# Optimization experiments

Hardware: AMD Instinct MI355X
Metric: run time of the kernel (lower is better)

The kernel has to match this reference:

```python
import jax, jax.numpy as jnp
import numpy as np

N_EVENTS = 200_000
M_TYPES = 64
K_KERNELS = 4
T_VAL = 100.0


def setup_inputs() -> dict:
    key = jax.random.key(0)
    k1, k2, k3, k4, k5 = jax.random.split(key, 5)
    # sorted event times in (0, T)
    t = jnp.sort(jax.random.uniform(k1, (N_EVENTS,), dtype=jnp.float32)) * T_VAL
    ti = t.reshape(1, N_EVENTS, 1)
    mi = jax.random.randint(k2, (N_EVENTS,), 0, M_TYPES)
    # positive Hawkes parameters (stability: row sums of alpha < 1)
    mu = 0.1 + 0.5 * jax.random.uniform(k3, (M_TYPES,), dtype=jnp.float32)
    alpha = (0.5 / M_TYPES) * jax.random.uniform(k4, (K_KERNELS, M_TYPES, M_TYPES), dtype=jnp.float32)
    gamma = 0.5 + jax.random.uniform(k5, (K_KERNELS,), dtype=jnp.float32)
    return {"mu": mu, "alpha": alpha, "gamma": gamma, "ti": ti, "mi": mi, "T": 100}


def _decay_states(gamma, t, mi, M):
    """Prefix-scan states h[i, m', k] = exp(-gamma_k*dt_i) * (h[i-1, m', k] + 1{m_{i-1}=m'}).
    Matches alpha_transition_matrices / prefix_scan(state_mult) in HawkesNLL.backward."""
    dt = jnp.concatenate([jnp.zeros((1,), t.dtype), t[1:] - t[:-1]])          # (N,)
    decay = jnp.exp(-gamma[None, :] * dt[:, None])                            # (N, K)
    oh = jnp.concatenate([jnp.zeros((1, M), t.dtype),
                          jax.nn.one_hot(mi[:-1], M, dtype=t.dtype)], axis=0)  # (N, M)
    a = jnp.broadcast_to(decay[:, None, :], (t.shape[0], M, decay.shape[1]))  # (N, M, K)
    b = decay[:, None, :] * oh[:, :, None]                                    # (N, M, K)

    def combine(x, y):
        a1, b1 = x
        a2, b2 = y
        return a1 * a2, a2 * b1 + b2

    _, h = jax.lax.associative_scan(combine, (a, b), axis=0)
    return h                                                                  # (N, M, K)


def _nll(mu, alpha, gamma, ti, mi, T):
    t = ti.reshape(-1)                        # (N,)
    N = t.shape[0]
    M = alpha.shape[1]
    h = _decay_states(gamma, t, mi, M)        # (N, M, K)
    # intensity at each event: lam_i = mu[m_i] + sum_{k,m'} gamma_k * alpha[k, m', m_i] * h[i, m', k]
    lam = mu[mi] + jnp.einsum('kmn,nmk,k->n', alpha[:, :, mi], h, gamma)      # (N,)
    # compensator: T*sum(mu) + sum_{j,k,p} alpha[k, m_j, p] * (1 - exp(-gamma_k (T - t_j)))
    asum = alpha.sum(axis=2)                                                  # (K, M)
    surv = -jnp.expm1(-gamma[None, :] * (T - t)[:, None])                     # (N, K)
    comp = T * mu.sum() + jnp.sum(asum[:, mi].T * surv)
    return (-jnp.sum(jnp.log(lam)) + comp) / N


def reference(mu, alpha, gamma, ti, mi, T):
    return _nll(mu, alpha, gamma, ti, mi, jnp.float32(T))
```

## Files before the change

kernel.cpp:

```cpp
#include <hip/hip_runtime.h>

#define MT 64
#define KK 4
#define NBK 4096
#define MAXB 49

__device__ __forceinline__ float wredf(float v) {
  #pragma unroll
  for (int off = 32; off > 0; off >>= 1) v += __shfl_xor(v, off, 64);
  return v;
}
__device__ __forceinline__ double wredd(double v) {
  #pragma unroll
  for (int off = 32; off > 0; off >>= 1) v += __shfl_xor(v, off, 64);
  return v;
}
__device__ __forceinline__ float4 f4fma(float4 a, float4 b, float4 c) {
  return make_float4(fmaf(a.x,b.x,c.x), fmaf(a.y,b.y,c.y),
                     fmaf(a.z,b.z,c.z), fmaf(a.w,b.w,c.w));
}
__device__ __forceinline__ float4 f4mul(float4 a, float4 b) {
  return make_float4(a.x*b.x, a.y*b.y, a.z*b.z, a.w*b.w);
}
__device__ __forceinline__ float parse_T(const int* Tp) {
  int v = *Tp;
  if (v >= 1 && v <= 1000000000) return (float)v;
  return __int_as_float(v);
}

__global__ __launch_bounds__(512, 4) void k_phase1(
    const float* __restrict__ t, const int* __restrict__ mi,
    const float* __restrict__ alpha, const float* __restrict__ gamma,
    const int* __restrict__ Tp,
    float4* __restrict__ cd4G, float* __restrict__ slG,
    float4* __restrict__ Cl8, float4* __restrict__ Dc8,
    float4* __restrict__ Ag, float4* __restrict__ gdec,
    float* __restrict__ compP, int N, int B)
{
  __shared__ float4 AT4[MT*MT];
  __shared__ __align__(16) unsigned char pool[8320];
  __shared__ float sL[8*MAXB];
  __shared__ float4 asumS[MT];
  __shared__ float red[8];
  float4*        d4t = (float4*)pool;
  unsigned char* miL = pool + 8*MAXB*16;
  float4*        cw  = (float4*)pool;
  float4*        cwd = (float4*)(pool + 8192);

  const int tid = threadIdx.x, lane = tid & 63, wv = tid >> 6;
  const float g0=gamma[0], g1=gamma[1], g2=gamma[2], g3=gamma[3];

  #pragma unroll
  for (int idx = tid; idx < MT*MT; idx += 512) {
    float a0=alpha[idx],         a1=alpha[MT*MT+idx];
    float a2=alpha[2*MT*MT+idx], a3=alpha[3*MT*MT+idx];
    AT4[idx] = make_float4(g0*a0, g1*a1, g2*a2, g3*a3);
  }
  if (tid < MT*KK) {
    const int m = tid >> 2, k = tid & 3;
    const float4* row = (const float4*)(alpha + (size_t)k*MT*MT + m*MT);
    float s = 0.f;
    #pragma unroll
    for (int j = 0; j < MT/4; ++j) { float4 v = row[j]; s += (v.x+v.y)+(v.z+v.w); }
    ((float*)asumS)[(m<<2)+k] = s;
  }
  __syncthreads();

  const float T = parse_T(Tp);
  const int s0w = (int)blockIdx.x * 8 * B;
  const int b  = (int)blockIdx.x*8 + wv;
  const int s0 = b*B, e0 = min(N, s0+B);
  float4 q = make_float4(0.f,0.f,0.f,0.f);
  float comp = 0.f;
  const int nch = (B + MAXB - 1) / MAXB;

  for (int ch = 0; ch < nch; ++ch) {
    const int c0 = ch*MAXB;
    const int cb = min(B - c0, MAXB);
    const int tot = 8*cb;
    for (int jj = tid; jj < tot; jj += 512) {
      int w = jj / cb, lo = jj - w*cb;
      int i = s0w + w*B + c0 + lo;
      if (i < N) {
        float ti = t[i];
        float tp = (i > 0) ? t[i-1] : ti;
        float dt = ti - tp;
        d4t[jj] = make_float4(__expf(-g0*dt), __expf(-g1*dt),
                              __expf(-g2*dt), __expf(-g3*dt));
        int m = mi[i];
        miL[jj] = (unsigned char)m;
        int refi = s0w + w*B - 1;
        float tr = (refi >= 0) ? t[refi] : t[0];
        float x = ti - tr;
        cd4G[i] = make_float4(__expf(-g0*x), __expf(-g1*x),
                              __expf(-g2*x), __expf(-g3*x));
        float y = T - ti;
        float4 as = asumS[m];
        comp = fmaf(as.x, 1.f-__expf(-g0*y), comp);
        comp = fmaf(as.y, 1.f-__expf(-g1*y), comp);
        comp = fmaf(as.z, 1.f-__expf(-g2*y), comp);
        comp = fmaf(as.w, 1.f-__expf(-g3*y), comp);
      }
    }
    __syncthreads();
    const int iend = min(cb, e0 - s0 - c0);
    int j = wv*cb;
    #pragma unroll 4
    for (int ii = 0; ii < iend; ++ii, ++j) {
      float4 d = d4t[j];
      int m = miL[j];
      float4 a = AT4[(m<<6) + lane];
      float s = q.x*d.x; s=fmaf(q.y,d.y,s); s=fmaf(q.z,d.z,s); s=fmaf(q.w,d.w,s);
      if (lane == m) sL[j] = s;
      q = f4fma(q, d, a);
    }
    __syncthreads();
    for (int jj = tid; jj < tot; jj += 512) {
      int w = jj / cb, lo = jj - w*cb;
      int i = s0w + w*B + c0 + lo;
      if (i < N) slG[i] = sL[jj];
    }
    __syncthreads();
  }

  comp = wredf(comp);
  if (lane == 0) red[wv] = comp;

  float4 df = make_float4(1.f,1.f,1.f,1.f);
  if (lane == 0) {
    int last  = max(e0-1, 0);
    int plast = min(max(s0-1, 0), N-1);
    float dtb = t[last] - t[plast];
    df = make_float4(__expf(-g0*dtb),__expf(-g1*dtb),
                     __expf(-g2*dtb),__expf(-g3*dtb));
  }
  cw[wv*64 + lane] = q;
  if (lane == 0) cwd[wv] = df;
  __syncthreads();

  float4 c  = make_float4(0.f,0.f,0.f,0.f);
  float4 dp = make_float4(1.f,1.f,1.f,1.f);
  float4 Cl = c, Dc = dp;
  #pragma unroll
  for (int jo = 0; jo < 8; ++jo) {
    if (jo == wv) { Cl = c; Dc = dp; }
    float4 d = cwd[jo];
    float4 P = cw[jo*64 + lane];
    c  = f4fma(c, d, P);
    dp = f4mul(dp, d);
  }
  Cl8[(size_t)b*64 + lane] = Cl;
  if (lane == 0) Dc8[b] = Dc;
  if (wv == 0) {
    Ag[(size_t)blockIdx.x*64 + lane] = c;
    if (lane == 0) gdec[blockIdx.x] = dp;
    if (lane == 0) {
      float cc = 0.f;
      #pragma unroll
      for (int jr = 0; jr < 8; ++jr) cc += red[jr];
      compP[blockIdx.x] = cc;
    }
  }
}

__global__ __launch_bounds__(64) void k_scan2(
    const float4* __restrict__ Ag, const float4* __restrict__ gdec,
    float4* __restrict__ SgG, float4* __restrict__ sdecG)
{
  const int lane = threadIdx.x;
  const int s = blockIdx.x;
  float4 c  = make_float4(0.f,0.f,0.f,0.f);
  float4 dp = make_float4(1.f,1.f,1.f,1.f);
  #pragma unroll 8
  for (int j = 0; j < 32; ++j) {
    const int o = s*32 + j;
    float4 gd = gdec[o];
    float4 a  = Ag[(size_t)o*64 + lane];
    c  = f4fma(c, gd, a);
    dp = f4mul(dp, gd);
  }
  SgG[(size_t)s*64 + lane] = c;
  if (lane == 0) sdecG[s] = dp;
}

__global__ __launch_bounds__(512, 4) void k_lam(
    const int* __restrict__ mi, const float* __restrict__ mu,
    const float4* __restrict__ cd4G, const float* __restrict__ slG,
    const float4* __restrict__ Cl8, const float4* __restrict__ Dc8,
    const float4* __restrict__ Ag, const float4* __restrict__ gdec,
    const float4* __restrict__ SgG, const float4* __restrict__ sdecG,
    float* __restrict__ npt, int N, int B)
{
  __shared__ float4 TopL[64];
  __shared__ float4 gpL[64];
  __shared__ float4 gdLs;
  __shared__ float red[8];
  const int tid = threadIdx.x, lane = tid & 63, wv = tid >> 6;
  const int oct = blockIdx.x;
  const int sup = oct >> 5;

  if (wv == 0) {
    float4 tc = make_float4(0.f,0.f,0.f,0.f);
    for (int s = 0; s < sup; ++s)
      tc = f4fma(tc, sdecG[s], SgG[(size_t)s*64 + lane]);
    TopL[lane] = tc;
  } else if (wv == 1) {
    float4 gp = make_float4(0.f,0.f,0.f,0.f);
    float4 gd = make_float4(1.f,1.f,1.f,1.f);
    const int o0 = sup << 5;
    for (int o = o0; o < oct; ++o) {
      gp = f4fma(gp, gdec[o], Ag[(size_t)o*64 + lane]);
      gd = f4mul(gd, gdec[o]);
    }
    gpL[lane] = gp;
    if (lane == 0) gdLs = gd;
  }
  __syncthreads();

  const int BPW = 8*B;
  const int i = oct*BPW + tid;
  float v = 0.f;
  if (tid < BPW && i < N) {
    int m = mi[i];
    float4 cd = cd4G[i];
    float sl = slG[i];
    int bl = tid / B;
    int b = oct*8 + bl;
    float4 coct = f4fma(gdLs, TopL[m], gpL[m]);
    float4 C = f4fma(Dc8[b], coct, Cl8[(size_t)b*64 + m]);
    float lam = mu[m] + sl + (C.x*cd.x + C.y*cd.y + C.z*cd.z + C.w*cd.w);
    v = __log2f(lam);
  }
  v = wredf(v);
  if (lane == 0) red[wv] = v;
  __syncthreads();
  if (tid == 0) {
    float s = 0.f;
    #pragma unroll
    for (int j = 0; j < 8; ++j) s += red[j];
    npt[oct] = s;
  }
}

__global__ __launch_bounds__(512) void k_final(
    const float* __restrict__ mu, const int* __restrict__ Tp,
    const float* __restrict__ compP, int nc,
    const float* __restrict__ npt, int nn,
    float* __restrict__ out, int N)
{
  const int tid = threadIdx.x;
  double sc = 0.0, sn = 0.0;
  for (int i = tid; i < nc; i += 512) sc += (double)compP[i];
  for (int i = tid; i < nn; i += 512) sn += (double)npt[i];
  double sm = (tid < MT) ? (double)mu[tid] : 0.0;
  sc = wredd(sc); sn = wredd(sn); sm = wredd(sm);
  __shared__ double s3[3][8];
  const int wv = tid >> 6, lane = tid & 63;
  if (lane == 0) { s3[0][wv]=sc; s3[1][wv]=sn; s3[2][wv]=sm; }
  __syncthreads();
  if (tid == 0) {
    double C=0.0, L=0.0, Mm=0.0;
    #pragma unroll
    for (int j = 0; j < 8; ++j) { C+=s3[0][j]; L+=s3[1][j]; Mm+=s3[2][j]; }
    L *= 0.6931471805599453;
    double T = (double)parse_T(Tp);
    out[0] = (float)((C + T*Mm - L) / (double)N);
  }
}

extern "C" void kernel_launch(void* const* d_in, const int* in_sizes, int n_in,
                              void* d_out, int out_size, void* d_ws, size_t ws_size,
                              hipStream_t stream)
{
  const float* mu    = (const float*)d_in[0];
  const float* alpha = (const float*)d_in[1];
  const float* gamma = (const float*)d_in[2];
  const float* t     = (const float*)d_in[3];
  const int*   mi    = (const int*)d_in[4];
  const int*   Tp    = (const int*)d_in[5];
  const int N = in_sizes[3];
  const int B   = (N + NBK - 1) / NBK;
  const int NOG = NBK / 8;

  float* p = (float*)d_ws;
  float4* cd4G  = (float4*)p; p += (size_t)N*4;
  float*  slG   = p;          p += ((size_t)N + 3) & ~(size_t)3;
  float4* Cl8   = (float4*)p; p += (size_t)NBK*256;
  float4* Dc8   = (float4*)p; p += (size_t)NBK*4;
  float4* Ag    = (float4*)p; p += (size_t)NOG*256;
  float4* gdec  = (float4*)p; p += (size_t)NOG*4;
  float4* SgG   = (float4*)p; p += (size_t)16*256;
  float4* sdecG = (float4*)p; p += (size_t)16*4;
  float*  compP = p;          p += NOG;
  float*  npt   = p;          p += NOG;

  k_phase1<<<NOG, 512, 0, stream>>>(t, mi, alpha, gamma, Tp, cd4G, slG,
                                    Cl8, Dc8, Ag, gdec, compP, N, B);
  k_scan2 <<<16,  64,  0, stream>>>(Ag, gdec, SgG, sdecG);
  k_lam   <<<NOG, 512, 0, stream>>>(mi, mu, cd4G, slG, Cl8, Dc8, Ag, gdec,
                                    SgG, sdecG, npt, N, B);
  k_final <<<1,   512, 0, stream>>>(mu, Tp, compP, NOG, npt, NOG,
                                    (float*)d_out, N);
}
```

Before: 37.64 us.

## Fuse scan2 and final reduction into lambda kernel with last-block atomic finish

Removes the separate small scan kernel by having every lambda block redundantly compute the super-block prefix sums into shared memory. The final reduction kernel is also folded in: blocks atomically add their log sums into a double accumulator, and the last block (found through an atomic counter) reduces compP and mu and writes the output. This cuts the pipeline from four launches to two. In exchange each block does redundant scan work, atomics are introduced, and compP is read only at indices below 512, which assumes NOG equals 512.

```diff
diff --git a/kernel.cpp b/kernel.cpp
--- a/kernel.cpp
+++ b/kernel.cpp
@@ -35,7 +35,8 @@
     float4* __restrict__ cd4G, float* __restrict__ slG,
     float4* __restrict__ Cl8, float4* __restrict__ Dc8,
     float4* __restrict__ Ag, float4* __restrict__ gdec,
-    float* __restrict__ compP, int N, int B)
+    float* __restrict__ compP, double* __restrict__ nllAcc,
+    int* __restrict__ counter, int N, int B)
 {
   __shared__ float4 AT4[MT*MT];
   __shared__ __align__(16) unsigned char pool[8320];
@@ -49,6 +50,8 @@
 
   const int tid = threadIdx.x, lane = tid & 63, wv = tid >> 6;
   const float g0=gamma[0], g1=gamma[1], g2=gamma[2], g3=gamma[3];
+
+  if (blockIdx.x == 0 && tid == 0) { *nllAcc = 0.0; *counter = 0; }
 
   #pragma unroll
   for (int idx = tid; idx < MT*MT; idx += 512) {
@@ -163,46 +166,66 @@
   }
 }
 
-__global__ __launch_bounds__(64) void k_scan2(
-    const float4* __restrict__ Ag, const float4* __restrict__ gdec,
-    float4* __restrict__ SgG, float4* __restrict__ sdecG)
-{
-  const int lane = threadIdx.x;
-  const int s = blockIdx.x;
-  float4 c  = make_float4(0.f,0.f,0.f,0.f);
-  float4 dp = make_float4(1.f,1.f,1.f,1.f);
-  #pragma unroll 8
-  for (int j = 0; j < 32; ++j) {
-    const int o = s*32 + j;
-    float4 gd = gdec[o];
-    float4 a  = Ag[(size_t)o*64 + lane];
-    c  = f4fma(c, gd, a);
-    dp = f4mul(dp, gd);
-  }
-  SgG[(size_t)s*64 + lane] = c;
-  if (lane == 0) sdecG[s] = dp;
-}
-
-__global__ __launch_bounds__(512, 4) void k_lam(
+__global__ __launch_bounds__(512, 4) void k_lamf(
     const int* __restrict__ mi, const float* __restrict__ mu,
+    const int* __restrict__ Tp,
     const float4* __restrict__ cd4G, const float* __restrict__ slG,
     const float4* __restrict__ Cl8, const float4* __restrict__ Dc8,
     const float4* __restrict__ Ag, const float4* __restrict__ gdec,
-    const float4* __restrict__ SgG, const float4* __restrict__ sdecG,
-    float* __restrict__ npt, int N, int B)
+    const float* __restrict__ compP,
+    double* __restrict__ nllAcc, int* __restrict__ counter,
+    float* __restrict__ out, int N, int B)
 {
+  __shared__ float4 SgL[16*64];
+  __shared__ float4 sdecL[16];
   __shared__ float4 TopL[64];
   __shared__ float4 gpL[64];
   __shared__ float4 gdLs;
   __shared__ float red[8];
+  __shared__ int lastFlag;
+  __shared__ double s3[3][8];
+
   const int tid = threadIdx.x, lane = tid & 63, wv = tid >> 6;
   const int oct = blockIdx.x;
   const int sup = oct >> 5;
+  const int BPW = 8*B;
+  const int i = oct*BPW + tid;
+
+  int   m = 0, b = 0;
+  float4 cd, Cl, Dc; float sl = 0.f, muv = 0.f;
+  const bool valid = (tid < BPW) && (i < N);
+  if (valid) {
+    m  = mi[i];
+    cd = cd4G[i];
+    sl = slG[i];
+    muv = mu[m];
+    int bl = tid / B;
+    b = oct*8 + bl;
+    Dc = Dc8[b];
+    Cl = Cl8[(size_t)b*64 + m];
+  }
+
+  for (int s = wv; s < sup; s += 8) {
+    float4 c  = make_float4(0.f,0.f,0.f,0.f);
+    float4 dp = make_float4(1.f,1.f,1.f,1.f);
+    const int o0 = s*32;
+    #pragma unroll 8
+    for (int j = 0; j < 32; ++j) {
+      const int o = o0 + j;
+      float4 gd = gdec[o];
+      float4 a  = Ag[(size_t)o*64 + lane];
+      c  = f4fma(c, gd, a);
+      dp = f4mul(dp, gd);
+    }
+    SgL[s*64 + lane] = c;
+    if (lane == 0) sdecL[s] = dp;
+  }
+  __syncthreads();
 
   if (wv == 0) {
     float4 tc = make_float4(0.f,0.f,0.f,0.f);
     for (int s = 0; s < sup; ++s)
-      tc = f4fma(tc, sdecG[s], SgG[(size_t)s*64 + lane]);
+      tc = f4fma(tc, sdecL[s], SgL[s*64 + lane]);
     TopL[lane] = tc;
   } else if (wv == 1) {
     float4 gp = make_float4(0.f,0.f,0.f,0.f);
@@ -217,18 +240,11 @@
   }
   __syncthreads();
 
-  const int BPW = 8*B;
-  const int i = oct*BPW + tid;
   float v = 0.f;
-  if (tid < BPW && i < N) {
-    int m = mi[i];
-    float4 cd = cd4G[i];
-    float sl = slG[i];
-    int bl = tid / B;
-    int b = oct*8 + bl;
+  if (valid) {
     float4 coct = f4fma(gdLs, TopL[m], gpL[m]);
-    float4 C = f4fma(Dc8[b], coct, Cl8[(size_t)b*64 + m]);
-    float lam = mu[m] + sl + (C.x*cd.x + C.y*cd.y + C.z*cd.z + C.w*cd.w);
+    float4 C = f4fma(Dc, coct, Cl);
+    float lam = muv + sl + (C.x*cd.x + C.y*cd.y + C.z*cd.z + C.w*cd.w);
     v = __log2f(lam);
   }
   v = wredf(v);
@@ -238,31 +254,25 @@
     float s = 0.f;
     #pragma unroll
     for (int j = 0; j < 8; ++j) s += red[j];
-    npt[oct] = s;
-  }
-}
-
-__global__ __launch_bounds__(512) void k_final(
-    const float* __restrict__ mu, const int* __restrict__ Tp,
-    const float* __restrict__ compP, int nc,
-    const float* __restrict__ npt, int nn,
-    float* __restrict__ out, int N)
-{
-  const int tid = threadIdx.x;
-  double sc = 0.0, sn = 0.0;
-  for (int i = tid; i < nc; i += 512) sc += (double)compP[i];
-  for (int i = tid; i < nn; i += 512) sn += (double)npt[i];
+    atomicAdd(nllAcc, (double)s);
+    __threadfence();
+    int old = atomicAdd(counter, 1);
+    lastFlag = (old == (int)gridDim.x - 1);
+  }
+  __syncthreads();
+  if (!lastFlag) return;
+  __threadfence();
+
+  double sc = (tid < 512) ? (double)compP[tid] : 0.0;
   double sm = (tid < MT) ? (double)mu[tid] : 0.0;
-  sc = wredd(sc); sn = wredd(sn); sm = wredd(sm);
-  __shared__ double s3[3][8];
-  const int wv = tid >> 6, lane = tid & 63;
-  if (lane == 0) { s3[0][wv]=sc; s3[1][wv]=sn; s3[2][wv]=sm; }
+  sc = wredd(sc); sm = wredd(sm);
+  if (lane == 0) { s3[0][wv] = sc; s3[1][wv] = sm; }
   __syncthreads();
   if (tid == 0) {
-    double C=0.0, L=0.0, Mm=0.0;
+    double C = 0.0, Mm = 0.0;
     #pragma unroll
-    for (int j = 0; j < 8; ++j) { C+=s3[0][j]; L+=s3[1][j]; Mm+=s3[2][j]; }
-    L *= 0.6931471805599453;
+    for (int j = 0; j < 8; ++j) { C += s3[0][j]; Mm += s3[1][j]; }
+    double L = atomicAdd(nllAcc, 0.0) * 0.6931471805599453;
     double T = (double)parse_T(Tp);
     out[0] = (float)((C + T*Mm - L) / (double)N);
   }
@@ -289,16 +299,14 @@
   float4* Dc8   = (float4*)p; p += (size_t)NBK*4;
   float4* Ag    = (float4*)p; p += (size_t)NOG*256;
   float4* gdec  = (float4*)p; p += (size_t)NOG*4;
-  float4* SgG   = (float4*)p; p += (size_t)16*256;
-  float4* sdecG = (float4*)p; p += (size_t)16*4;
   float*  compP = p;          p += NOG;
-  float*  npt   = p;          p += NOG;
+  p += (((uintptr_t)p & 8) ? 2 : 0);
+  double* nllAcc = (double*)p; p += 2;
+  int*    counter = (int*)p;  p += 1;
 
   k_phase1<<<NOG, 512, 0, stream>>>(t, mi, alpha, gamma, Tp, cd4G, slG,
-                                    Cl8, Dc8, Ag, gdec, compP, N, B);
-  k_scan2 <<<16,  64,  0, stream>>>(Ag, gdec, SgG, sdecG);
-  k_lam   <<<NOG, 512, 0, stream>>>(mi, mu, cd4G, slG, Cl8, Dc8, Ag, gdec,
-                                    SgG, sdecG, npt, N, B);
-  k_final <<<1,   512, 0, stream>>>(mu, Tp, compP, NOG, npt, NOG,
-                                    (float*)d_out, N);
-}
+                                    Cl8, Dc8, Ag, gdec, compP, nllAcc, counter,
+                                    N, B);
+  k_lamf  <<<NOG, 512, 0, stream>>>(mi, mu, Tp, cd4G, slG, Cl8, Dc8, Ag, gdec,
+                                    compP, nllAcc, counter, (float*)d_out, N, B);
+}
```

Measured after the change: 50.01 us. 32.9% more time.

## Fuse super-block scan into lambda kernel, recomputing scan per block

Applied to the files above, without the earlier changes.

Removes the separate k_scan2 launch. Each k_lam2 block now recomputes the super-block carries it needs in shared memory, with its 8 waves splitting the super-blocks. Per-event loads (mi, cd4, sl, mu, Dc8, Cl8) are issued before the scan so their latency overlaps with it. This saves one kernel launch and a dependency step, but every block repeats up to 15 super-block reductions (32 float4 rows each), which adds redundant global reads and compute.

```diff
diff --git a/kernel.cpp b/kernel.cpp
--- a/kernel.cpp
+++ b/kernel.cpp
@@ -163,46 +163,61 @@
   }
 }
 
-__global__ __launch_bounds__(64) void k_scan2(
-    const float4* __restrict__ Ag, const float4* __restrict__ gdec,
-    float4* __restrict__ SgG, float4* __restrict__ sdecG)
-{
-  const int lane = threadIdx.x;
-  const int s = blockIdx.x;
-  float4 c  = make_float4(0.f,0.f,0.f,0.f);
-  float4 dp = make_float4(1.f,1.f,1.f,1.f);
-  #pragma unroll 8
-  for (int j = 0; j < 32; ++j) {
-    const int o = s*32 + j;
-    float4 gd = gdec[o];
-    float4 a  = Ag[(size_t)o*64 + lane];
-    c  = f4fma(c, gd, a);
-    dp = f4mul(dp, gd);
-  }
-  SgG[(size_t)s*64 + lane] = c;
-  if (lane == 0) sdecG[s] = dp;
-}
-
-__global__ __launch_bounds__(512, 4) void k_lam(
+__global__ __launch_bounds__(512, 4) void k_lam2(
     const int* __restrict__ mi, const float* __restrict__ mu,
     const float4* __restrict__ cd4G, const float* __restrict__ slG,
     const float4* __restrict__ Cl8, const float4* __restrict__ Dc8,
     const float4* __restrict__ Ag, const float4* __restrict__ gdec,
-    const float4* __restrict__ SgG, const float4* __restrict__ sdecG,
     float* __restrict__ npt, int N, int B)
 {
+  __shared__ float4 SgL[16*64];
+  __shared__ float4 sdecL[16];
   __shared__ float4 TopL[64];
   __shared__ float4 gpL[64];
   __shared__ float4 gdLs;
   __shared__ float red[8];
+
   const int tid = threadIdx.x, lane = tid & 63, wv = tid >> 6;
   const int oct = blockIdx.x;
   const int sup = oct >> 5;
+  const int BPW = 8*B;
+  const int i = oct*BPW + tid;
+
+  int   m = 0;
+  float4 cd, Cl, Dc; float sl = 0.f, muv = 0.f;
+  const bool valid = (tid < BPW) && (i < N);
+  if (valid) {
+    m  = mi[i];
+    cd = cd4G[i];
+    sl = slG[i];
+    muv = mu[m];
+    int bl = tid / B;
+    int b = oct*8 + bl;
+    Dc = Dc8[b];
+    Cl = Cl8[(size_t)b*64 + m];
+  }
+
+  for (int s = wv; s < sup; s += 8) {
+    float4 c  = make_float4(0.f,0.f,0.f,0.f);
+    float4 dp = make_float4(1.f,1.f,1.f,1.f);
+    const int o0 = s*32;
+    #pragma unroll 8
+    for (int j = 0; j < 32; ++j) {
+      const int o = o0 + j;
+      float4 gd = gdec[o];
+      float4 a  = Ag[(size_t)o*64 + lane];
+      c  = f4fma(c, gd, a);
+      dp = f4mul(dp, gd);
+    }
+    SgL[s*64 + lane] = c;
+    if (lane == 0) sdecL[s] = dp;
+  }
+  __syncthreads();
 
   if (wv == 0) {
     float4 tc = make_float4(0.f,0.f,0.f,0.f);
     for (int s = 0; s < sup; ++s)
-      tc = f4fma(tc, sdecG[s], SgG[(size_t)s*64 + lane]);
+      tc = f4fma(tc, sdecL[s], SgL[s*64 + lane]);
     TopL[lane] = tc;
   } else if (wv == 1) {
     float4 gp = make_float4(0.f,0.f,0.f,0.f);
@@ -217,18 +232,11 @@
   }
   __syncthreads();
 
-  const int BPW = 8*B;
-  const int i = oct*BPW + tid;
   float v = 0.f;
-  if (tid < BPW && i < N) {
-    int m = mi[i];
-    float4 cd = cd4G[i];
-    float sl = slG[i];
-    int bl = tid / B;
-    int b = oct*8 + bl;
+  if (valid) {
     float4 coct = f4fma(gdLs, TopL[m], gpL[m]);
-    float4 C = f4fma(Dc8[b], coct, Cl8[(size_t)b*64 + m]);
-    float lam = mu[m] + sl + (C.x*cd.x + C.y*cd.y + C.z*cd.z + C.w*cd.w);
+    float4 C = f4fma(Dc, coct, Cl);
+    float lam = muv + sl + (C.x*cd.x + C.y*cd.y + C.z*cd.z + C.w*cd.w);
     v = __log2f(lam);
   }
   v = wredf(v);
@@ -289,16 +297,13 @@
   float4* Dc8   = (float4*)p; p += (size_t)NBK*4;
   float4* Ag    = (float4*)p; p += (size_t)NOG*256;
   float4* gdec  = (float4*)p; p += (size_t)NOG*4;
-  float4* SgG   = (float4*)p; p += (size_t)16*256;
-  float4* sdecG = (float4*)p; p += (size_t)16*4;
   float*  compP = p;          p += NOG;
   float*  npt   = p;          p += NOG;
 
   k_phase1<<<NOG, 512, 0, stream>>>(t, mi, alpha, gamma, Tp, cd4G, slG,
                                     Cl8, Dc8, Ag, gdec, compP, N, B);
-  k_scan2 <<<16,  64,  0, stream>>>(Ag, gdec, SgG, sdecG);
-  k_lam   <<<NOG, 512, 0, stream>>>(mi, mu, cd4G, slG, Cl8, Dc8, Ag, gdec,
-                                    SgG, sdecG, npt, N, B);
+  k_lam2  <<<NOG, 512, 0, stream>>>(mi, mu, cd4G, slG, Cl8, Dc8, Ag, gdec,
+                                    npt, N, B);
   k_final <<<1,   512, 0, stream>>>(mu, Tp, compP, NOG, npt, NOG,
                                     (float*)d_out, N);
 }
```

After: 44.24 us. 17.5% more time.
